# Performance work log

Hardware: AMD Instinct MI355X
Metric: run time of the kernel (lower is better)

## Reference

```python
import jax, jax.numpy as jnp
import numpy as np

TRANSFORMATION_WEIGHT = 0.01


def setup_inputs() -> dict:
    key = jax.random.key(0)
    k1, k2 = jax.random.split(key)
    B, N, M, D = 4, 8192, 8192, 3
    return {
        "transformed_source": jax.random.normal(k1, (B, N, D), dtype=jnp.float32),
        "transformed_target": jax.random.normal(k2, (B, M, D), dtype=jnp.float32),
    }


def reference(transformed_source, transformed_target):
    # Chamfer distance (pytorch3d defaults: squared L2, point mean, batch mean)
    x = transformed_source.astype(jnp.float32)  # [B, N, 3]
    y = transformed_target.astype(jnp.float32)  # [B, M, 3]
    x2 = jnp.sum(x * x, axis=-1)                # [B, N]
    y2 = jnp.sum(y * y, axis=-1)                # [B, M]
    xy = jnp.einsum("bnd,bmd->bnm", x, y)       # [B, N, M]
    d2 = x2[:, :, None] + y2[:, None, :] - 2.0 * xy  # squared pairwise dists
    cham_x = jnp.mean(jnp.min(d2, axis=2))      # source -> target NN, mean over points & batch
    cham_y = jnp.mean(jnp.min(d2, axis=1))      # target -> source NN
    transformation_loss = cham_x + cham_y
    return TRANSFORMATION_WEIGHT * transformation_loss
```

## Files before the change

kernel.cpp:

```cpp
#include <hip/hip_runtime.h>

#define BB 4
#define NN 8192
#define INF_BITS 0x7f7f7f7fu

typedef __attribute__((ext_vector_type(8)))  short bf16x8;
typedef __attribute__((ext_vector_type(16))) float f32x16;


__device__ __forceinline__ unsigned short bf_hi(float f) {
    unsigned u = __float_as_uint(f);
    u += 0x7fffu + ((u >> 16) & 1u);
    return (unsigned short)(u >> 16);
}

__global__ __launch_bounds__(256) void prep_kernel(
        const float* __restrict__ s, const float* __restrict__ t,
        bf16x8* __restrict__ sApk, bf16x8* __restrict__ sBpk,
        bf16x8* __restrict__ tApk, bf16x8* __restrict__ tBpk,
        float* __restrict__ snorm, float* __restrict__ tnorm,
        unsigned* __restrict__ minb) {
    int i = blockIdx.x * 256 + threadIdx.x;
    int set = i >> 15;
    int p = i & 32767;
    const float* in = set ? t : s;
    float x = in[3*p], y = in[3*p+1], z = in[3*p+2];

    unsigned short xh = bf_hi(x); float fxh = __uint_as_float((unsigned)xh << 16);
    unsigned short yh = bf_hi(y); float fyh = __uint_as_float((unsigned)yh << 16);
    unsigned short zh = bf_hi(z); float fzh = __uint_as_float((unsigned)zh << 16);
    unsigned short xl = bf_hi(x - fxh);
    unsigned short yl = bf_hi(y - fyh);
    unsigned short zl = bf_hi(z - fzh);
    float fxl = __uint_as_float((unsigned)xl << 16);
    float fyl = __uint_as_float((unsigned)yl << 16);
    float fzl = __uint_as_float((unsigned)zl << 16);
    unsigned short mxh = bf_hi(-2.0f*fxh), mxl = bf_hi(-2.0f*fxl);
    unsigned short myh = bf_hi(-2.0f*fyh), myl = bf_hi(-2.0f*fyl);
    unsigned short mzh = bf_hi(-2.0f*fzh), mzl = bf_hi(-2.0f*fzl);

    float n = x*x + y*y + z*z;
    unsigned short nh = bf_hi(n); float fnh = __uint_as_float((unsigned)nh << 16);
    unsigned short nl = bf_hi(n - fnh);
    const short one = (short)0x3F80;

    bf16x8 alo = {(short)mxh,(short)mxl,(short)mxh,(short)myh,(short)myl,(short)myh,(short)mzh,(short)mzl};
    bf16x8 ahi = {(short)mzh,(short)nh,(short)nl,0,0,0,0,0};
    bf16x8 blo = {(short)xh,(short)xh,(short)xl,(short)yh,(short)yh,(short)yl,(short)zh,(short)zh};
    bf16x8 bhi = {(short)zl,one,one,0,0,0,0,0};

    bf16x8* A = set ? tApk : sApk;
    bf16x8* B = set ? tBpk : sBpk;
    int tile = p >> 5, l = p & 31;
    A[tile*64 + l]      = alo;
    A[tile*64 + 32 + l] = ahi;
    B[tile*64 + l]      = blo;
    B[tile*64 + 32 + l] = bhi;

    (set ? tnorm : snorm)[p] = n;
    minb[i] = INF_BITS;
}

__device__ __forceinline__ void tile_step(const bf16x8& A0, const bf16x8& A1,
                                          const bf16x8* Bf, f32x16* run, const f32x16& cz) {
#pragma unroll
    for (int t = 0; t < 4; ++t) {
        f32x16 aA = __builtin_amdgcn_mfma_f32_32x32x16_bf16(A0, Bf[t], cz, 0, 0, 0);
        f32x16 aB = __builtin_amdgcn_mfma_f32_32x32x16_bf16(A1, Bf[t], cz, 0, 0, 0);
#pragma unroll
        for (int i = 0; i < 16; ++i)
            run[t][i] = fminf(fminf(aA[i], aB[i]), run[t][i]);
    }
}

__global__ __launch_bounds__(64) void minpass_kernel(
        const bf16x8* __restrict__ sApk, const bf16x8* __restrict__ sBpk,
        const bf16x8* __restrict__ tApk, const bf16x8* __restrict__ tBpk,
        const float* __restrict__ snorm, const float* __restrict__ tnorm,
        unsigned* __restrict__ minb) {
    int bid = blockIdx.x;
    int tc  = bid & 7;
    int sg  = (bid >> 3) & 63;
    int b   = (bid >> 9) & 3;
    int dir = bid >> 11;

    const bf16x8* Ap = dir ? sApk : tApk;
    const bf16x8* Bp = dir ? tBpk : sBpk;
    const float*  nrm = dir ? tnorm : snorm;
    unsigned* out = minb + dir * (BB * NN) + b * NN;

    int lane = threadIdx.x;

    bf16x8 Bf[4];
#pragma unroll
    for (int t = 0; t < 4; ++t)
        Bf[t] = Bp[(b * 256 + sg * 4 + t) * 64 + lane];

    f32x16 run[4];
#pragma unroll
    for (int t = 0; t < 4; ++t)
#pragma unroll
        for (int i = 0; i < 16; ++i) run[t][i] = 3.0e38f;

    f32x16 cz = {};

    const bf16x8* Abase = Ap + (b * 256 + tc * 32) * 64 + lane;
    bf16x8 A0 = Abase[0];
    bf16x8 A1 = Abase[64];
#pragma unroll 1
    for (int j = 0; j < 30; j += 2) {
        bf16x8 N0 = Abase[(j + 2) * 64];
        bf16x8 N1 = Abase[(j + 3) * 64];
        tile_step(A0, A1, Bf, run, cz);
        A0 = N0; A1 = N1;
    }
    tile_step(A0, A1, Bf, run, cz);

#pragma unroll
    for (int t = 0; t < 4; ++t) {
        f32x16 r = run[t];
        float a0 = fminf(r[0], r[8]),  a1 = fminf(r[1], r[9]);
        float a2 = fminf(r[2], r[10]), a3 = fminf(r[3], r[11]);
        float a4 = fminf(a0, fminf(r[4], r[12])), a5 = fminf(a1, fminf(r[5], r[13]));
        float a6 = fminf(a2, fminf(r[6], r[14])), a7 = fminf(a3, fminf(r[7], r[15]));
        float m  = fminf(fminf(a4, a5), fminf(a6, a7));
        m = fminf(m, __shfl_xor(m, 32));
        int src = (sg * 4 + t) * 32 + (lane & 31);
        float val = fmaxf(m + nrm[b * NN + src], 0.0f);
        if (lane < 32)
            atomicMin(out + src, __float_as_uint(val));
    }
}

__global__ __launch_bounds__(1024) void finalize_kernel(const uint4* __restrict__ minb4,
                                                        float* __restrict__ out) {
    float s0 = 0.f, s1 = 0.f;
    for (int i = threadIdx.x; i < 8192; i += 1024) {
        uint4 u = minb4[i];
        s0 += __uint_as_float(u.x) + __uint_as_float(u.y) +
              __uint_as_float(u.z) + __uint_as_float(u.w);
        uint4 v = minb4[8192 + i];
        s1 += __uint_as_float(v.x) + __uint_as_float(v.y) +
              __uint_as_float(v.z) + __uint_as_float(v.w);
    }
#pragma unroll
    for (int o = 32; o; o >>= 1) {
        s0 += __shfl_down(s0, o);
        s1 += __shfl_down(s1, o);
    }
    __shared__ float r0[16], r1[16];
    int wave = threadIdx.x >> 6;
    if ((threadIdx.x & 63) == 0) { r0[wave] = s0; r1[wave] = s1; }
    __syncthreads();
    if (threadIdx.x == 0) {
        float a = 0.f, c = 0.f;
#pragma unroll
        for (int w = 0; w < 16; ++w) { a += r0[w]; c += r1[w]; }
        out[0] = 0.01f * (a / (float)(BB * NN) + c / (float)(BB * NN));
    }
}

extern "C" void kernel_launch(void* const* d_in, const int* in_sizes, int n_in,
                              void* d_out, int out_size, void* d_ws, size_t ws_size,
                              hipStream_t stream) {
    const float* s = (const float*)d_in[0];
    const float* t = (const float*)d_in[1];

    bf16x8* sApk = (bf16x8*)d_ws;
    bf16x8* sBpk = sApk + 65536;
    bf16x8* tApk = sBpk + 65536;
    bf16x8* tBpk = tApk + 65536;
    float*  snorm = (float*)(tBpk + 65536);
    float*  tnorm = snorm + 32768;
    unsigned* minb = (unsigned*)(tnorm + 32768);

    prep_kernel<<<256, 256, 0, stream>>>(s, t, sApk, sBpk, tApk, tBpk, snorm, tnorm, minb);
    minpass_kernel<<<4096, 64, 0, stream>>>(sApk, sBpk, tApk, tBpk, snorm, tnorm, minb);
    finalize_kernel<<<1, 1024, 0, stream>>>((const uint4*)minb, (float*)d_out);
}
```

Baseline: 40.22 us.

## Halve per-block B tiles, double grid, use v_min3 and deeper A prefetch

Measured after the change: 39.73 us. Within noise of the previous version (-1.2%).

```diff
diff --git a/kernel.cpp b/kernel.cpp
--- a/kernel.cpp
+++ b/kernel.cpp
@@ -12,6 +12,12 @@
     unsigned u = __float_as_uint(f);
     u += 0x7fffu + ((u >> 16) & 1u);
     return (unsigned short)(u >> 16);
+}
+
+__device__ __forceinline__ float min3f(float a, float b, float c) {
+    float d;
+    asm("v_min3_f32 %0, %1, %2, %3" : "=v"(d) : "v"(a), "v"(b), "v"(c));
+    return d;
 }
 
 __global__ __launch_bounds__(256) void prep_kernel(
@@ -61,18 +67,6 @@
     minb[i] = INF_BITS;
 }
 
-__device__ __forceinline__ void tile_step(const bf16x8& A0, const bf16x8& A1,
-                                          const bf16x8* Bf, f32x16* run, const f32x16& cz) {
-#pragma unroll
-    for (int t = 0; t < 4; ++t) {
-        f32x16 aA = __builtin_amdgcn_mfma_f32_32x32x16_bf16(A0, Bf[t], cz, 0, 0, 0);
-        f32x16 aB = __builtin_amdgcn_mfma_f32_32x32x16_bf16(A1, Bf[t], cz, 0, 0, 0);
-#pragma unroll
-        for (int i = 0; i < 16; ++i)
-            run[t][i] = fminf(fminf(aA[i], aB[i]), run[t][i]);
-    }
-}
-
 __global__ __launch_bounds__(64) void minpass_kernel(
         const bf16x8* __restrict__ sApk, const bf16x8* __restrict__ sBpk,
         const bf16x8* __restrict__ tApk, const bf16x8* __restrict__ tBpk,
@@ -80,9 +74,9 @@
         unsigned* __restrict__ minb) {
     int bid = blockIdx.x;
     int tc  = bid & 7;
-    int sg  = (bid >> 3) & 63;
-    int b   = (bid >> 9) & 3;
-    int dir = bid >> 11;
+    int sg  = (bid >> 3) & 127;
+    int b   = (bid >> 10) & 3;
+    int dir = bid >> 12;
 
     const bf16x8* Ap = dir ? sApk : tApk;
     const bf16x8* Bp = dir ? tBpk : sBpk;
@@ -91,41 +85,59 @@
 
     int lane = threadIdx.x;
 
-    bf16x8 Bf[4];
+    bf16x8 Bf0 = Bp[(b * 256 + sg * 2 + 0) * 64 + lane];
+    bf16x8 Bf1 = Bp[(b * 256 + sg * 2 + 1) * 64 + lane];
+
+    f32x16 run0, run1;
 #pragma unroll
-    for (int t = 0; t < 4; ++t)
-        Bf[t] = Bp[(b * 256 + sg * 4 + t) * 64 + lane];
-
-    f32x16 run[4];
-#pragma unroll
-    for (int t = 0; t < 4; ++t)
-#pragma unroll
-        for (int i = 0; i < 16; ++i) run[t][i] = 3.0e38f;
+    for (int i = 0; i < 16; ++i) { run0[i] = 3.0e38f; run1[i] = 3.0e38f; }
 
     f32x16 cz = {};
 
-    const bf16x8* Abase = Ap + (b * 256 + tc * 32) * 64 + lane;
-    bf16x8 A0 = Abase[0];
-    bf16x8 A1 = Abase[64];
+    const bf16x8* Ab = Ap + (b * 256 + tc * 32) * 64 + lane;
+
+    bf16x8 C0 = Ab[0],   C1 = Ab[64];
+    bf16x8 P0 = Ab[128], P1 = Ab[192];
 #pragma unroll 1
-    for (int j = 0; j < 30; j += 2) {
-        bf16x8 N0 = Abase[(j + 2) * 64];
-        bf16x8 N1 = Abase[(j + 3) * 64];
-        tile_step(A0, A1, Bf, run, cz);
-        A0 = N0; A1 = N1;
+    for (int jp = 0; jp < 14; ++jp) {
+        bf16x8 N0 = Ab[(2 * jp + 4) * 64];
+        bf16x8 N1 = Ab[(2 * jp + 5) * 64];
+        f32x16 q0 = __builtin_amdgcn_mfma_f32_32x32x16_bf16(C0, Bf0, cz, 0, 0, 0);
+        f32x16 q1 = __builtin_amdgcn_mfma_f32_32x32x16_bf16(C1, Bf0, cz, 0, 0, 0);
+#pragma unroll
+        for (int i = 0; i < 16; ++i) run0[i] = min3f(q0[i], q1[i], run0[i]);
+        f32x16 r0 = __builtin_amdgcn_mfma_f32_32x32x16_bf16(C0, Bf1, cz, 0, 0, 0);
+        f32x16 r1 = __builtin_amdgcn_mfma_f32_32x32x16_bf16(C1, Bf1, cz, 0, 0, 0);
+#pragma unroll
+        for (int i = 0; i < 16; ++i) run1[i] = min3f(r0[i], r1[i], run1[i]);
+        C0 = P0; C1 = P1; P0 = N0; P1 = N1;
     }
-    tile_step(A0, A1, Bf, run, cz);
+#pragma unroll
+    for (int e = 0; e < 2; ++e) {
+        f32x16 q0 = __builtin_amdgcn_mfma_f32_32x32x16_bf16(C0, Bf0, cz, 0, 0, 0);
+        f32x16 q1 = __builtin_amdgcn_mfma_f32_32x32x16_bf16(C1, Bf0, cz, 0, 0, 0);
+#pragma unroll
+        for (int i = 0; i < 16; ++i) run0[i] = min3f(q0[i], q1[i], run0[i]);
+        f32x16 r0 = __builtin_amdgcn_mfma_f32_32x32x16_bf16(C0, Bf1, cz, 0, 0, 0);
+        f32x16 r1 = __builtin_amdgcn_mfma_f32_32x32x16_bf16(C1, Bf1, cz, 0, 0, 0);
+#pragma unroll
+        for (int i = 0; i < 16; ++i) run1[i] = min3f(r0[i], r1[i], run1[i]);
+        C0 = P0; C1 = P1;
+    }
 
 #pragma unroll
-    for (int t = 0; t < 4; ++t) {
-        f32x16 r = run[t];
-        float a0 = fminf(r[0], r[8]),  a1 = fminf(r[1], r[9]);
-        float a2 = fminf(r[2], r[10]), a3 = fminf(r[3], r[11]);
-        float a4 = fminf(a0, fminf(r[4], r[12])), a5 = fminf(a1, fminf(r[5], r[13]));
-        float a6 = fminf(a2, fminf(r[6], r[14])), a7 = fminf(a3, fminf(r[7], r[15]));
-        float m  = fminf(fminf(a4, a5), fminf(a6, a7));
+    for (int t = 0; t < 2; ++t) {
+        const f32x16& r = t ? run1 : run0;
+        float g0 = min3f(r[0],  r[1],  r[2]);
+        float g1 = min3f(r[3],  r[4],  r[5]);
+        float g2 = min3f(r[6],  r[7],  r[8]);
+        float g3 = min3f(r[9],  r[10], r[11]);
+        float g4 = min3f(r[12], r[13], r[14]);
+        float h0 = min3f(g0, g1, g2);
+        float h1 = min3f(g3, g4, r[15]);
+        float m  = fminf(h0, h1);
         m = fminf(m, __shfl_xor(m, 32));
-        int src = (sg * 4 + t) * 32 + (lane & 31);
+        int src = sg * 64 + t * 32 + (lane & 31);
         float val = fmaxf(m + nrm[b * NN + src], 0.0f);
         if (lane < 32)
             atomicMin(out + src, __float_as_uint(val));
@@ -175,6 +187,6 @@
     unsigned* minb = (unsigned*)(tnorm + 32768);
 
     prep_kernel<<<256, 256, 0, stream>>>(s, t, sApk, sBpk, tApk, tBpk, snorm, tnorm, minb);
-    minpass_kernel<<<4096, 64, 0, stream>>>(sApk, sBpk, tApk, tBpk, snorm, tnorm, minb);
+    minpass_kernel<<<2 * 4 * 128 * 8, 64, 0, stream>>>(sApk, sBpk, tApk, tBpk, snorm, tnorm, minb);
     finalize_kernel<<<1, 1024, 0, stream>>>((const uint4*)minb, (float*)d_out);
 }
```
